# Kernel tuning notes

Measured on AMD Instinct MI355X. Metric: run time of the kernel, lower is better.

The kernel has to match this reference:

```python
import jax, jax.numpy as jnp
import numpy as np

B = 65536
N_HOSTS = 16
N_FEATS = 48        # 3 * n_hosts
N_WINDOW = 3
N_LATENT = 10
GAT_IN = 3
GAT_OUT = 16
E = N_WINDOW + GAT_OUT  # 19, MHA embed dim
PROTO_DIM = 10


def setup_inputs() -> dict:
    key = jax.random.key(0)
    ks = jax.random.split(key, 20)
    def rn(k, shape, scale=0.1):
        return jax.random.normal(k, shape, dtype=jnp.float32) * scale
    return {
        "t": jax.random.normal(ks[0], (B, N_WINDOW, N_FEATS), dtype=jnp.float32),
        "s": jnp.zeros((1,), jnp.float32),  # unused by forward, kept for signature fidelity
        "h0": jax.random.normal(ks[1], (B, 1, N_WINDOW), dtype=jnp.float32),
        "gru_Wih": rn(ks[2], (3 * N_WINDOW, N_FEATS)),
        "gru_Whh": rn(ks[3], (3 * N_WINDOW, N_WINDOW)),
        "gru_bih": rn(ks[4], (3 * N_WINDOW,)),
        "gru_bhh": rn(ks[5], (3 * N_WINDOW,)),
        "gat_W": rn(ks[6], (GAT_IN, GAT_OUT)),
        "gat_al": rn(ks[7], (GAT_OUT,)),
        "gat_ar": rn(ks[8], (GAT_OUT,)),
        "mha_Win": rn(ks[9], (3 * E, E)),
        "mha_bin": rn(ks[10], (3 * E,)),
        "mha_Wout": rn(ks[11], (E, E)),
        "mha_bout": rn(ks[12], (E,)),
        "enc_W": rn(ks[13], (N_HOSTS * N_LATENT, N_WINDOW * E)),
        "enc_b": rn(ks[14], (N_HOSTS * N_LATENT,)),
        "anom_W": rn(ks[15], (2, N_LATENT)),
        "anom_b": rn(ks[16], (2,)),
        "proto_W": rn(ks[17], (PROTO_DIM, N_LATENT)),
        "proto_b": rn(ks[18], (PROTO_DIM,)),
    }


def _forward(t, s, h0, gru_Wih, gru_Whh, gru_bih, gru_bhh,
             gat_W, gat_al, gat_ar, mha_Win, mha_bin, mha_Wout, mha_bout,
             enc_W, enc_b, anom_W, anom_b, proto_W, proto_b):
    # ---- GRU (seq-first, batch B, hidden = n_window = 3) ----
    xs = jnp.swapaxes(t, 0, 1)  # (3, B, 48)
    h0_ = h0[:, 0, :]           # (B, 3)

    def gru_step(h, x_t):
        gi = x_t @ gru_Wih.T + gru_bih   # (B, 9)
        gh = h @ gru_Whh.T + gru_bhh     # (B, 9)
        i_r, i_z, i_n = jnp.split(gi, 3, axis=-1)
        h_r, h_z, h_n = jnp.split(gh, 3, axis=-1)
        r = jax.nn.sigmoid(i_r + h_r)
        z = jax.nn.sigmoid(i_z + h_z)
        n = jnp.tanh(i_n + r * h_n)
        h_new = (1.0 - z) * n + z * h
        return h_new, h_new

    _, gru_out = jax.lax.scan(gru_step, h0_, xs)  # (3, B, 3)

    # ---- GAT on fully-connected 16-node graph (with self loops) ----
    gin = t.reshape(t.shape[0], N_WINDOW, N_HOSTS, GAT_IN)      # (B, 3, 16, 3)
    z = jnp.einsum("bwnc,cf->bwnf", gin, gat_W)                 # (B, 3, 16, 16)
    el = z @ gat_al                                              # src scores (B,3,16)
    er = z @ gat_ar                                              # dst scores (B,3,16)
    e = jax.nn.leaky_relu(er[..., :, None] + el[..., None, :], 0.2)  # (B,3,v,u)
    alpha = jax.nn.softmax(e, axis=-1)                           # softmax over sources u
    gat_nodes = jnp.einsum("bwvu,bwuf->bwvf", alpha, z)          # (B, 3, 16, 16)
    gat_out = gat_nodes.mean(axis=2)                             # (B, 3, 16) mean over hosts
    gat_out = jnp.swapaxes(gat_out, 0, 1)                        # (3, B, 16)

    # ---- concat + single-head MHA (embed=19) ----
    c = jnp.concatenate([gru_out, gat_out], axis=-1)             # (3, B, 19)
    Wq, Wk, Wv = jnp.split(mha_Win, 3, axis=0)
    bq, bk, bv = jnp.split(mha_bin, 3, axis=0)
    q = c @ Wq.T + bq
    k = c @ Wk.T + bk
    v = c @ Wv.T + bv
    scores = jnp.einsum("sbe,tbe->bst", q, k) / jnp.sqrt(jnp.float32(E))
    attw = jax.nn.softmax(scores, axis=-1)
    attn = jnp.einsum("bst,tbe->sbe", attw, v)
    attn = attn @ mha_Wout.T + mha_bout                          # (3, B, 19)

    # ---- encoder: Linear(57,160); LeakyReLU(True) => negative_slope=1.0 => identity ----
    flat = jnp.swapaxes(attn, 0, 1).reshape(-1, N_WINDOW * E)    # (B, 57), seq-major flatten
    latent = flat @ enc_W.T + enc_b                              # (B, 160)
    latent = latent.reshape(-1, N_HOSTS, N_LATENT)               # (B, 16, 10)

    # ---- per-host tiny decoders, vectorized ----
    anomaly = jax.nn.softmax(latent @ anom_W.T + anom_b, axis=-1)   # (B, 16, 2)
    proto = jax.nn.sigmoid(latent @ proto_W.T + proto_b)            # (B, 16, PROTO_DIM)
    return anomaly, proto


def reference(t, s, h0, gru_Wih, gru_Whh, gru_bih, gru_bhh,
              gat_W, gat_al, gat_ar, mha_Win, mha_bin, mha_Wout, mha_bout,
              enc_W, enc_b, anom_W, anom_b, proto_W, proto_b):
    return _forward(t, s, h0, gru_Wih, gru_Whh, gru_bih, gru_bhh,
                    gat_W, gat_al, gat_ar, mha_Win, mha_bin, mha_Wout, mha_bout,
                    enc_W, enc_b, anom_W, anom_b, proto_W, proto_b)
```

## Files before the change

### kernel.cpp

```cpp
#include <hip/hip_runtime.h>

#define NW 3
#define NF 48
#define NHOST 16
#define NLAT 10
#define GOUT 16
#define EDIM 19
#define PDIM 10

#define CB_M    0
#define CB_P    361
#define CB_G    722
#define CB_H    741
#define CB_R    760
#define CB_C0   779
#define CB_WAL  780
#define CB_WAR  783
#define CB_CBIG 800
#define CB_BF   976
#define CB_TOT  10240

typedef __attribute__((ext_vector_type(8))) short bf16x8;
typedef __attribute__((ext_vector_type(4))) float f32x4;

__device__ __forceinline__ float frcp(float x){ return __builtin_amdgcn_rcpf(x); }
__device__ __forceinline__ float fsig(float x){ return frcp(1.f + __expf(-x)); }
__device__ __forceinline__ float ftanh(float x){ return 1.f - 2.f*frcp(1.f + __expf(2.f*x)); }
__device__ __forceinline__ unsigned short f2bf(float x){
    union { float f; unsigned u; } v; v.f = x;
    unsigned r = v.u + 0x7FFFu + ((v.u >> 16) & 1u);
    return (unsigned short)(r >> 16);
}

__global__ __launch_bounds__(256) void k_const(
    const float* __restrict__ Win, const float* __restrict__ bin,
    const float* __restrict__ Wout, const float* __restrict__ bout,
    const float* __restrict__ gatW, const float* __restrict__ gal,
    const float* __restrict__ gar, const float* __restrict__ encW,
    const float* __restrict__ encb,
    const float* __restrict__ aW, const float* __restrict__ ab,
    const float* __restrict__ pW, const float* __restrict__ pb,
    float* __restrict__ cb)
{
    const int w = blockIdx.x*blockDim.x + threadIdx.x;
    if (w < 786) {
        const int idx = w;
        float acc = 0.f;
        if (idx < 361) {
            int i = idx/19, j = idx%19;
            for (int e = 0; e < EDIM; ++e) acc += Win[e*EDIM+i]*Win[(EDIM+e)*EDIM+j];
        } else if (idx < 722) {
            int k = idx-361; int i = k/19, j = k%19;
            for (int e = 0; e < EDIM; ++e) acc += Wout[i*EDIM+e]*Win[(2*EDIM+e)*EDIM+j];
        } else if (idx < 741) {
            int j = idx-722;
            for (int e = 0; e < EDIM; ++e) acc += bin[e]*Win[(EDIM+e)*EDIM+j];
        } else if (idx < 760) {
            int i = idx-741;
            for (int e = 0; e < EDIM; ++e) acc += Win[e*EDIM+i]*bin[EDIM+e];
        } else if (idx < 779) {
            int i = idx-760; acc = bout[i];
            for (int e = 0; e < EDIM; ++e) acc += Wout[i*EDIM+e]*bin[2*EDIM+e];
        } else if (idx == 779) {
            for (int e = 0; e < EDIM; ++e) acc += bin[e]*bin[EDIM+e];
        } else {
            int c = idx-780; int cc = c%3; bool left = c<3;
            for (int f2 = 0; f2 < GOUT; ++f2)
                acc += gatW[cc*GOUT+f2]*(left ? gal[f2] : gar[f2]);
        }
        cb[idx] = acc;
    } else if (w < 962) {
        const int g = w - 786;
        int host = g / 11, jj = g % 11;
        float acc = (jj == 0) ? (ab[0] - ab[1]) : pb[jj-1];
        for (int l = 0; l < NLAT; ++l) {
            float coef = (jj == 0) ? (aW[l] - aW[NLAT+l]) : pW[(jj-1)*NLAT + l];
            acc += coef * encb[host*NLAT + l];
        }
        cb[CB_CBIG + g] = acc;
    } else if (w < 12226) {
        unsigned short* bf = (unsigned short*)(cb + CB_BF);
        const int u = w - 962;
        int j    = u & 7;
        int lane = (u >> 3) & 63;
        int tile = u >> 9;
        int half = tile / 11, n = tile % 11;
        int k = half*32 + ((lane >> 4) & 3)*8 + j;
        int g = n*16 + (lane & 15);
        float acc = 0.f;
        if (k < 57) {
            int host = g / 11, jj = g % 11;
            for (int l = 0; l < NLAT; ++l) {
                float coef = (jj == 0) ? (aW[l] - aW[NLAT+l]) : pW[(jj-1)*NLAT + l];
                acc += coef * encW[(host*NLAT + l)*57 + k];
            }
        }
        bf[u] = f2bf(acc);
    }
}

__global__ __launch_bounds__(256) void k_front(
    const float* __restrict__ t, const float* __restrict__ Wih, const float* __restrict__ bih,
    const float* __restrict__ gatW, const float* __restrict__ cb,
    float* __restrict__ ws1, int B)
{
    const int b = blockIdx.x*blockDim.x + threadIdx.x;
    const int w = blockIdx.y;
    if (b >= B) return;

    float x[NF];
    const float* tp = t + ((size_t)b*NW + w)*NF;
#pragma unroll
    for (int i = 0; i < NF/4; ++i) {
        float4 v = *reinterpret_cast<const float4*>(tp + i*4);
        x[i*4+0]=v.x; x[i*4+1]=v.y; x[i*4+2]=v.z; x[i*4+3]=v.w;
    }
    float* o = ws1 + (size_t)w*25*B + b;
#pragma unroll
    for (int r = 0; r < 9; ++r) {
        float acc = bih[r];
#pragma unroll
        for (int j = 0; j < NF; ++j) acc += x[j]*Wih[r*NF+j];
        o[(size_t)r*B] = acc;
    }
    const float Wal0=cb[CB_WAL],Wal1=cb[CB_WAL+1],Wal2=cb[CB_WAL+2];
    const float War0=cb[CB_WAR],War1=cb[CB_WAR+1],War2=cb[CB_WAR+2];
    float el[NHOST], er[NHOST];
#pragma unroll
    for (int n = 0; n < NHOST; ++n) {
        el[n] = x[n*3+0]*Wal0 + x[n*3+1]*Wal1 + x[n*3+2]*Wal2;
        er[n] = x[n*3+0]*War0 + x[n*3+1]*War1 + x[n*3+2]*War2;
    }
    float beta[NHOST];
#pragma unroll
    for (int u = 0; u < NHOST; ++u) beta[u] = 0.f;
#pragma unroll
    for (int v = 0; v < NHOST; ++v) {
        float ee[NHOST]; float sum = 0.f;
#pragma unroll
        for (int u = 0; u < NHOST; ++u) {
            float s = er[v] + el[u];
            s = fmaxf(s, 0.2f*s);
            ee[u] = __expf(s); sum += ee[u];
        }
        float inv = frcp(sum);
#pragma unroll
        for (int u = 0; u < NHOST; ++u) beta[u] += ee[u]*inv;
    }
    float g0=0.f, g1=0.f, g2=0.f;
#pragma unroll
    for (int u = 0; u < NHOST; ++u) {
        float bu = beta[u]*(1.f/16.f);
        g0 += bu*x[u*3+0]; g1 += bu*x[u*3+1]; g2 += bu*x[u*3+2];
    }
#pragma unroll
    for (int f2 = 0; f2 < GOUT; ++f2)
        o[(size_t)(9+f2)*B] = g0*gatW[f2] + g1*gatW[GOUT+f2] + g2*gatW[2*GOUT+f2];
}

__global__ __launch_bounds__(192) void k_m(
    const float* __restrict__ ws1, const float* __restrict__ h0,
    const float* __restrict__ Whh, const float* __restrict__ bhh,
    const float* __restrict__ cb, unsigned short* __restrict__ ws2bf, int B)
{
    __shared__ float mtb[NW][EDIM][64];
    __shared__ float gtb[NW][64];
    __shared__ float pcb[NW][EDIM][64];
    const int bl = threadIdx.x & 63;
    const int s  = threadIdx.x >> 6;
    const int b  = blockIdx.x*64 + bl;

    float h[3] = { h0[(size_t)b*3+0], h0[(size_t)b*3+1], h0[(size_t)b*3+2] };
    float ch[NW][3];
#pragma unroll
    for (int w = 0; w < NW; ++w) {
        float gi[9];
#pragma unroll
        for (int r = 0; r < 9; ++r) gi[r] = ws1[((size_t)w*25 + r)*B + b];
        float gh[9];
#pragma unroll
        for (int r = 0; r < 9; ++r)
            gh[r] = bhh[r] + h[0]*Whh[r*3+0] + h[1]*Whh[r*3+1] + h[2]*Whh[r*3+2];
#pragma unroll
        for (int j = 0; j < 3; ++j) {
            float rg = fsig(gi[j]   + gh[j]);
            float zg = fsig(gi[3+j] + gh[3+j]);
            float ng = ftanh(gi[6+j] + rg*gh[6+j]);
            h[j] = (1.f - zg)*ng + zg*h[j];
        }
        ch[w][0]=h[0]; ch[w][1]=h[1]; ch[w][2]=h[2];
    }
    float cw[EDIM];
#pragma unroll
    for (int j = 0; j < 3; ++j)
        cw[j] = (s==0) ? ch[0][j] : (s==1) ? ch[1][j] : ch[2][j];
#pragma unroll
    for (int f2 = 0; f2 < GOUT; ++f2)
        cw[3+f2] = ws1[((size_t)s*25 + 9 + f2)*B + b];

    float hsv = 0.f, gt = 0.f;
#pragma unroll
    for (int i = 0; i < EDIM; ++i) { hsv += cw[i]*cb[CB_H+i]; gt += cw[i]*cb[CB_G+i]; }
#pragma unroll
    for (int i = 0; i < EDIM; ++i) {
        float a = 0.f;
#pragma unroll
        for (int j = 0; j < EDIM; ++j) a += cb[CB_M+i*EDIM+j]*cw[j];
        mtb[s][i][bl] = a;
    }
    gtb[s][bl] = gt;
    __syncthreads();

    const float c0 = cb[CB_C0];
    float sc[NW];
#pragma unroll
    for (int tt = 0; tt < NW; ++tt) {
        float a = 0.f;
#pragma unroll
        for (int i = 0; i < EDIM; ++i) a += cw[i]*mtb[tt][i][bl];
        sc[tt] = (a + gtb[tt][bl] + hsv + c0) * 0.2294157338705618f;
    }
    float m = fmaxf(sc[0], fmaxf(sc[1], sc[2]));
    float e0=__expf(sc[0]-m), e1=__expf(sc[1]-m), e2=__expf(sc[2]-m);
    float inv = frcp(e0+e1+e2);
    float aw0=e0*inv, aw1=e1*inv, aw2=e2*inv;

#pragma unroll
    for (int i = 0; i < EDIM; ++i) {
        float a = 0.f;
#pragma unroll
        for (int j = 0; j < EDIM; ++j) a += cb[CB_P+i*EDIM+j]*cw[j];
        pcb[s][i][bl] = a;
    }
    __syncthreads();

    unsigned short* ob = ws2bf + (size_t)b*64 + s*EDIM;
#pragma unroll
    for (int i = 0; i < EDIM; ++i) {
        float v = cb[CB_R+i] + aw0*pcb[0][i][bl] + aw1*pcb[1][i][bl]
                + aw2*pcb[2][i][bl];
        ob[i] = f2bf(v);
    }
    if (s == 0) {
        unsigned short* pz = ws2bf + (size_t)b*64 + 57;
#pragma unroll
        for (int r = 0; r < 7; ++r) pz[r] = 0;
    }
}

__global__ __launch_bounds__(256) void k_enc(
    const unsigned short* __restrict__ ws2bf, const float* __restrict__ cb,
    float* __restrict__ outA, float* __restrict__ outP, int B)
{
    __shared__ float lg[64][178];
    const int lane = threadIdx.x & 63;
    const int wv   = __builtin_amdgcn_readfirstlane(threadIdx.x >> 6);
    const int b0   = blockIdx.x*64;
    if (b0 >= B) return;

    const int brow = b0 + wv*16 + (lane & 15);
    const int koff = (lane >> 4) * 8;
    const unsigned short* ap = ws2bf + (size_t)brow*64;
    union { uint4 q; bf16x8 v; } a0, a1;
    a0.q = *reinterpret_cast<const uint4*>(ap + koff);
    a1.q = *reinterpret_cast<const uint4*>(ap + 32 + koff);

    const uint4* bfq = (const uint4*)(cb + CB_BF);
    const int r0 = wv*16 + ((lane >> 4) << 2);
#pragma unroll
    for (int n = 0; n < 11; ++n) {
        union { uint4 q; bf16x8 v; } bf0, bf1;
        bf0.q = bfq[(size_t)n*64 + lane];
        bf1.q = bfq[(size_t)(11 + n)*64 + lane];
        f32x4 acc = {0.f, 0.f, 0.f, 0.f};
        acc = __builtin_amdgcn_mfma_f32_16x16x32_bf16(a0.v, bf0.v, acc, 0, 0, 0);
        acc = __builtin_amdgcn_mfma_f32_16x16x32_bf16(a1.v, bf1.v, acc, 0, 0, 0);
        const int c = n*16 + (lane & 15);
#pragma unroll
        for (int r = 0; r < 4; ++r) lg[r0 + r][c] = acc[r];
    }
    __syncthreads();

    const int host = threadIdx.x & 15;
    const int tg   = threadIdx.x >> 4;
    const float* cbig = cb + CB_CBIG;
#pragma unroll
    for (int i = 0; i < 4; ++i) {
        const int bl = tg + 16*i;
        const int b  = b0 + bl;
        float v[11];
#pragma unroll
        for (int jj = 0; jj < 11; ++jj)
            v[jj] = lg[bl][host*11 + jj] + cbig[host*11 + jj];
        float p0 = fsig(v[0]);
        float2 av; av.x = p0; av.y = 1.f - p0;
        *reinterpret_cast<float2*>(outA + (size_t)b*32 + host*2) = av;
        float* pP = outP + (size_t)b*160 + host*10;
#pragma unroll
        for (int p = 0; p < 5; ++p) {
            float2 pv; pv.x = fsig(v[1 + 2*p]); pv.y = fsig(v[2 + 2*p]);
            *reinterpret_cast<float2*>(pP + 2*p) = pv;
        }
    }
}

extern "C" void kernel_launch(void* const* d_in, const int* in_sizes, int n_in,
                              void* d_out, int out_size, void* d_ws, size_t ws_size,
                              hipStream_t stream) {
    const float* t    = (const float*)d_in[0];
    const float* h0   = (const float*)d_in[2];
    const float* Wih  = (const float*)d_in[3];
    const float* Whh  = (const float*)d_in[4];
    const float* bih  = (const float*)d_in[5];
    const float* bhh  = (const float*)d_in[6];
    const float* gatW = (const float*)d_in[7];
    const float* gal  = (const float*)d_in[8];
    const float* gar  = (const float*)d_in[9];
    const float* Win  = (const float*)d_in[10];
    const float* bin  = (const float*)d_in[11];
    const float* Wout = (const float*)d_in[12];
    const float* bout = (const float*)d_in[13];
    const float* encW = (const float*)d_in[14];
    const float* encb = (const float*)d_in[15];
    const float* aW   = (const float*)d_in[16];
    const float* ab   = (const float*)d_in[17];
    const float* pW   = (const float*)d_in[18];
    const float* pb   = (const float*)d_in[19];

    const int B = in_sizes[0] / (NW * NF);
    float* cb  = (float*)d_ws;
    float* ws1 = cb + CB_TOT;
    unsigned short* ws2bf = (unsigned short*)(ws1 + (size_t)25*NW*B);
    float* outA = (float*)d_out;
    float* outP = (float*)d_out + (size_t)B*32;

    k_const<<<dim3(48), 256, 0, stream>>>(Win, bin, Wout, bout, gatW, gal, gar,
                                          encW, encb, aW, ab, pW, pb, cb);
    k_front<<<dim3((B+255)/256, NW), 256, 0, stream>>>(t, Wih, bih, gatW, cb, ws1, B);
    k_m<<<dim3(B/64), 192, 0, stream>>>(ws1, h0, Whh, bhh, cb, ws2bf, B);
    k_enc<<<dim3((B+63)/64), 256, 0, stream>>>(ws2bf, cb, outA, outP, B);
}
```

Measured before the change: 73.20 us.

## Fuse front, attention, and encoder kernels into one block-local kernel

Merges the GRU/GAT front kernel, the attention kernel, and the MFMA encoder kernel into one kernel per 64-row tile. Intermediates move through LDS (with an XOR-swizzled bf16 A tile) instead of global workspace buffers. This removes two launches and the global round trips of the ws1 and ws2bf intermediates. In exchange it uses about 64KB of LDS per block, which limits occupancy, and a quarter of the threads sit idle during the front stages.

```diff
diff --git a/kernel.cpp b/kernel.cpp
--- a/kernel.cpp
+++ b/kernel.cpp
@@ -99,207 +99,239 @@
     }
 }
 
-__global__ __launch_bounds__(256) void k_front(
-    const float* __restrict__ t, const float* __restrict__ Wih, const float* __restrict__ bih,
-    const float* __restrict__ gatW, const float* __restrict__ cb,
-    float* __restrict__ ws1, int B)
-{
-    const int b = blockIdx.x*blockDim.x + threadIdx.x;
-    const int w = blockIdx.y;
-    if (b >= B) return;
-
-    float x[NF];
-    const float* tp = t + ((size_t)b*NW + w)*NF;
-#pragma unroll
-    for (int i = 0; i < NF/4; ++i) {
-        float4 v = *reinterpret_cast<const float4*>(tp + i*4);
-        x[i*4+0]=v.x; x[i*4+1]=v.y; x[i*4+2]=v.z; x[i*4+3]=v.w;
-    }
-    float* o = ws1 + (size_t)w*25*B + b;
-#pragma unroll
-    for (int r = 0; r < 9; ++r) {
-        float acc = bih[r];
-#pragma unroll
-        for (int j = 0; j < NF; ++j) acc += x[j]*Wih[r*NF+j];
-        o[(size_t)r*B] = acc;
-    }
-    const float Wal0=cb[CB_WAL],Wal1=cb[CB_WAL+1],Wal2=cb[CB_WAL+2];
-    const float War0=cb[CB_WAR],War1=cb[CB_WAR+1],War2=cb[CB_WAR+2];
-    float el[NHOST], er[NHOST];
-#pragma unroll
-    for (int n = 0; n < NHOST; ++n) {
-        el[n] = x[n*3+0]*Wal0 + x[n*3+1]*Wal1 + x[n*3+2]*Wal2;
-        er[n] = x[n*3+0]*War0 + x[n*3+1]*War1 + x[n*3+2]*War2;
-    }
-    float beta[NHOST];
-#pragma unroll
-    for (int u = 0; u < NHOST; ++u) beta[u] = 0.f;
-#pragma unroll
-    for (int v = 0; v < NHOST; ++v) {
-        float ee[NHOST]; float sum = 0.f;
-#pragma unroll
-        for (int u = 0; u < NHOST; ++u) {
-            float s = er[v] + el[u];
-            s = fmaxf(s, 0.2f*s);
-            ee[u] = __expf(s); sum += ee[u];
-        }
-        float inv = frcp(sum);
-#pragma unroll
-        for (int u = 0; u < NHOST; ++u) beta[u] += ee[u]*inv;
-    }
-    float g0=0.f, g1=0.f, g2=0.f;
-#pragma unroll
-    for (int u = 0; u < NHOST; ++u) {
-        float bu = beta[u]*(1.f/16.f);
-        g0 += bu*x[u*3+0]; g1 += bu*x[u*3+1]; g2 += bu*x[u*3+2];
-    }
-#pragma unroll
-    for (int f2 = 0; f2 < GOUT; ++f2)
-        o[(size_t)(9+f2)*B] = g0*gatW[f2] + g1*gatW[GOUT+f2] + g2*gatW[2*GOUT+f2];
-}
-
-__global__ __launch_bounds__(192) void k_m(
-    const float* __restrict__ ws1, const float* __restrict__ h0,
-    const float* __restrict__ Whh, const float* __restrict__ bhh,
-    const float* __restrict__ cb, unsigned short* __restrict__ ws2bf, int B)
-{
-    __shared__ float mtb[NW][EDIM][64];
-    __shared__ float gtb[NW][64];
-    __shared__ float pcb[NW][EDIM][64];
-    const int bl = threadIdx.x & 63;
-    const int s  = threadIdx.x >> 6;
-    const int b  = blockIdx.x*64 + bl;
-
-    float h[3] = { h0[(size_t)b*3+0], h0[(size_t)b*3+1], h0[(size_t)b*3+2] };
-    float ch[NW][3];
-#pragma unroll
-    for (int w = 0; w < NW; ++w) {
-        float gi[9];
-#pragma unroll
-        for (int r = 0; r < 9; ++r) gi[r] = ws1[((size_t)w*25 + r)*B + b];
-        float gh[9];
-#pragma unroll
-        for (int r = 0; r < 9; ++r)
-            gh[r] = bhh[r] + h[0]*Whh[r*3+0] + h[1]*Whh[r*3+1] + h[2]*Whh[r*3+2];
-#pragma unroll
-        for (int j = 0; j < 3; ++j) {
-            float rg = fsig(gi[j]   + gh[j]);
-            float zg = fsig(gi[3+j] + gh[3+j]);
-            float ng = ftanh(gi[6+j] + rg*gh[6+j]);
-            h[j] = (1.f - zg)*ng + zg*h[j];
-        }
-        ch[w][0]=h[0]; ch[w][1]=h[1]; ch[w][2]=h[2];
-    }
-    float cw[EDIM];
-#pragma unroll
-    for (int j = 0; j < 3; ++j)
-        cw[j] = (s==0) ? ch[0][j] : (s==1) ? ch[1][j] : ch[2][j];
-#pragma unroll
-    for (int f2 = 0; f2 < GOUT; ++f2)
-        cw[3+f2] = ws1[((size_t)s*25 + 9 + f2)*B + b];
-
-    float hsv = 0.f, gt = 0.f;
-#pragma unroll
-    for (int i = 0; i < EDIM; ++i) { hsv += cw[i]*cb[CB_H+i]; gt += cw[i]*cb[CB_G+i]; }
-#pragma unroll
-    for (int i = 0; i < EDIM; ++i) {
-        float a = 0.f;
-#pragma unroll
-        for (int j = 0; j < EDIM; ++j) a += cb[CB_M+i*EDIM+j]*cw[j];
-        mtb[s][i][bl] = a;
-    }
-    gtb[s][bl] = gt;
-    __syncthreads();
-
-    const float c0 = cb[CB_C0];
-    float sc[NW];
-#pragma unroll
-    for (int tt = 0; tt < NW; ++tt) {
-        float a = 0.f;
-#pragma unroll
-        for (int i = 0; i < EDIM; ++i) a += cw[i]*mtb[tt][i][bl];
-        sc[tt] = (a + gtb[tt][bl] + hsv + c0) * 0.2294157338705618f;
-    }
-    float m = fmaxf(sc[0], fmaxf(sc[1], sc[2]));
-    float e0=__expf(sc[0]-m), e1=__expf(sc[1]-m), e2=__expf(sc[2]-m);
-    float inv = frcp(e0+e1+e2);
-    float aw0=e0*inv, aw1=e1*inv, aw2=e2*inv;
-
-#pragma unroll
-    for (int i = 0; i < EDIM; ++i) {
-        float a = 0.f;
-#pragma unroll
-        for (int j = 0; j < EDIM; ++j) a += cb[CB_P+i*EDIM+j]*cw[j];
-        pcb[s][i][bl] = a;
-    }
-    __syncthreads();
-
-    unsigned short* ob = ws2bf + (size_t)b*64 + s*EDIM;
-#pragma unroll
-    for (int i = 0; i < EDIM; ++i) {
-        float v = cb[CB_R+i] + aw0*pcb[0][i][bl] + aw1*pcb[1][i][bl]
-                + aw2*pcb[2][i][bl];
-        ob[i] = f2bf(v);
-    }
-    if (s == 0) {
-        unsigned short* pz = ws2bf + (size_t)b*64 + 57;
-#pragma unroll
-        for (int r = 0; r < 7; ++r) pz[r] = 0;
-    }
-}
-
-__global__ __launch_bounds__(256) void k_enc(
-    const unsigned short* __restrict__ ws2bf, const float* __restrict__ cb,
+__global__ __launch_bounds__(256) void k_fused(
+    const float* __restrict__ t, const float* __restrict__ h0,
+    const float* __restrict__ Wih, const float* __restrict__ bih,
+    const float* __restrict__ gatW, const float* __restrict__ Whh,
+    const float* __restrict__ bhh, const float* __restrict__ cb,
     float* __restrict__ outA, float* __restrict__ outP, int B)
 {
-    __shared__ float lg[64][178];
-    const int lane = threadIdx.x & 63;
-    const int wv   = __builtin_amdgcn_readfirstlane(threadIdx.x >> 6);
-    const int b0   = blockIdx.x*64;
-    if (b0 >= B) return;
-
-    const int brow = b0 + wv*16 + (lane & 15);
-    const int koff = (lane >> 4) * 8;
-    const unsigned short* ap = ws2bf + (size_t)brow*64;
-    union { uint4 q; bf16x8 v; } a0, a1;
-    a0.q = *reinterpret_cast<const uint4*>(ap + koff);
-    a1.q = *reinterpret_cast<const uint4*>(ap + 32 + koff);
-
-    const uint4* bfq = (const uint4*)(cb + CB_BF);
-    const int r0 = wv*16 + ((lane >> 4) << 2);
-#pragma unroll
-    for (int n = 0; n < 11; ++n) {
-        union { uint4 q; bf16x8 v; } bf0, bf1;
-        bf0.q = bfq[(size_t)n*64 + lane];
-        bf1.q = bfq[(size_t)(11 + n)*64 + lane];
-        f32x4 acc = {0.f, 0.f, 0.f, 0.f};
-        acc = __builtin_amdgcn_mfma_f32_16x16x32_bf16(a0.v, bf0.v, acc, 0, 0, 0);
-        acc = __builtin_amdgcn_mfma_f32_16x16x32_bf16(a1.v, bf1.v, acc, 0, 0, 0);
-        const int c = n*16 + (lane & 15);
-#pragma unroll
-        for (int r = 0; r < 4; ++r) lg[r0 + r][c] = acc[r];
-    }
-    __syncthreads();
-
-    const int host = threadIdx.x & 15;
-    const int tg   = threadIdx.x >> 4;
-    const float* cbig = cb + CB_CBIG;
-#pragma unroll
-    for (int i = 0; i < 4; ++i) {
-        const int bl = tg + 16*i;
-        const int b  = b0 + bl;
-        float v[11];
-#pragma unroll
-        for (int jj = 0; jj < 11; ++jj)
-            v[jj] = lg[bl][host*11 + jj] + cbig[host*11 + jj];
-        float p0 = fsig(v[0]);
-        float2 av; av.x = p0; av.y = 1.f - p0;
-        *reinterpret_cast<float2*>(outA + (size_t)b*32 + host*2) = av;
-        float* pP = outP + (size_t)b*160 + host*10;
-#pragma unroll
-        for (int p = 0; p < 5; ++p) {
-            float2 pv; pv.x = fsig(v[1 + 2*p]); pv.y = fsig(v[2 + 2*p]);
-            *reinterpret_cast<float2*>(pP + 2*p) = pv;
+    __shared__ __align__(16) char smraw[57344];
+    __shared__ __align__(16) unsigned short a2[64][64];
+    float (*fm)[25][64] = reinterpret_cast<float(*)[25][64]>(smraw);
+    float* xs            = reinterpret_cast<float*>(smraw + 19200);
+    float (*mtb)[EDIM][64] = reinterpret_cast<float(*)[EDIM][64]>(smraw + 19200);
+    float (*gtb)[64]       = reinterpret_cast<float(*)[64]>(smraw + 19200 + 14592);
+    float (*pcb)[EDIM][64] = reinterpret_cast<float(*)[EDIM][64]>(smraw + 19200 + 15360);
+    float (*lg)[178]       = reinterpret_cast<float(*)[178]>(smraw);
+
+    const int tid = threadIdx.x;
+    const int b0  = blockIdx.x * 64;
+    const int bl  = tid & 63;
+    const int sw  = tid >> 6;
+
+    if (tid < 192) {
+        const int w = sw;
+        const float* tp = t + ((size_t)(b0 + bl)*NW + w)*NF;
+        float* xrow = xs + tid*49;
+
+        const float Wal0=cb[CB_WAL],Wal1=cb[CB_WAL+1],Wal2=cb[CB_WAL+2];
+        const float War0=cb[CB_WAR],War1=cb[CB_WAR+1],War2=cb[CB_WAR+2];
+
+        float gi[9];
+#pragma unroll
+        for (int r = 0; r < 9; ++r) gi[r] = bih[r];
+        float el[NHOST], er[NHOST];
+#pragma unroll
+        for (int c = 0; c < 4; ++c) {
+            float xc[12];
+#pragma unroll
+            for (int i = 0; i < 3; ++i) {
+                float4 v = *reinterpret_cast<const float4*>(tp + c*12 + i*4);
+                xc[i*4+0]=v.x; xc[i*4+1]=v.y; xc[i*4+2]=v.z; xc[i*4+3]=v.w;
+            }
+#pragma unroll
+            for (int k = 0; k < 12; ++k) xrow[c*12 + k] = xc[k];
+#pragma unroll
+            for (int r = 0; r < 9; ++r) {
+                float a = 0.f;
+#pragma unroll
+                for (int k = 0; k < 12; ++k) a += xc[k]*Wih[r*NF + c*12 + k];
+                gi[r] += a;
+            }
+#pragma unroll
+            for (int u = 0; u < 4; ++u) {
+                const int uu = c*4 + u;
+                el[uu] = xc[u*3]*Wal0 + xc[u*3+1]*Wal1 + xc[u*3+2]*Wal2;
+                er[uu] = xc[u*3]*War0 + xc[u*3+1]*War1 + xc[u*3+2]*War2;
+            }
+        }
+#pragma unroll
+        for (int r = 0; r < 9; ++r) fm[w][r][bl] = gi[r];
+
+        float beta[NHOST];
+#pragma unroll
+        for (int u = 0; u < NHOST; ++u) beta[u] = 0.f;
+#pragma unroll
+        for (int v = 0; v < NHOST; ++v) {
+            float ee[NHOST]; float sum = 0.f;
+#pragma unroll
+            for (int u = 0; u < NHOST; ++u) {
+                float s = er[v] + el[u];
+                s = fmaxf(s, 0.2f*s);
+                ee[u] = __expf(s); sum += ee[u];
+            }
+            float inv = frcp(sum);
+#pragma unroll
+            for (int u = 0; u < NHOST; ++u) beta[u] += ee[u]*inv;
+        }
+        float g0=0.f, g1=0.f, g2=0.f;
+#pragma unroll
+        for (int u = 0; u < NHOST; ++u) {
+            float bu = beta[u]*(1.f/16.f);
+            g0 += bu*xrow[u*3+0]; g1 += bu*xrow[u*3+1]; g2 += bu*xrow[u*3+2];
+        }
+#pragma unroll
+        for (int f2 = 0; f2 < GOUT; ++f2)
+            fm[w][9+f2][bl] = g0*gatW[f2] + g1*gatW[GOUT+f2] + g2*gatW[2*GOUT+f2];
+    }
+    __syncthreads();
+
+    float cw[EDIM];
+    float hsv = 0.f, aw0 = 0.f, aw1 = 0.f, aw2 = 0.f;
+#pragma unroll
+    for (int i = 0; i < EDIM; ++i) cw[i] = 0.f;
+
+    if (tid < 192) {
+        const int s = sw;
+        const int b = b0 + bl;
+        float h[3] = { h0[(size_t)b*3+0], h0[(size_t)b*3+1], h0[(size_t)b*3+2] };
+        float ch[NW][3];
+#pragma unroll
+        for (int w = 0; w < NW; ++w) {
+            float gi[9];
+#pragma unroll
+            for (int r = 0; r < 9; ++r) gi[r] = fm[w][r][bl];
+            float gh[9];
+#pragma unroll
+            for (int r = 0; r < 9; ++r)
+                gh[r] = bhh[r] + h[0]*Whh[r*3+0] + h[1]*Whh[r*3+1] + h[2]*Whh[r*3+2];
+#pragma unroll
+            for (int j = 0; j < 3; ++j) {
+                float rg = fsig(gi[j]   + gh[j]);
+                float zg = fsig(gi[3+j] + gh[3+j]);
+                float ng = ftanh(gi[6+j] + rg*gh[6+j]);
+                h[j] = (1.f - zg)*ng + zg*h[j];
+            }
+            ch[w][0]=h[0]; ch[w][1]=h[1]; ch[w][2]=h[2];
+        }
+#pragma unroll
+        for (int j = 0; j < 3; ++j)
+            cw[j] = (s==0) ? ch[0][j] : (s==1) ? ch[1][j] : ch[2][j];
+#pragma unroll
+        for (int f2 = 0; f2 < GOUT; ++f2)
+            cw[3+f2] = fm[s][9+f2][bl];
+
+        float gt = 0.f;
+#pragma unroll
+        for (int i = 0; i < EDIM; ++i) { hsv += cw[i]*cb[CB_H+i]; gt += cw[i]*cb[CB_G+i]; }
+#pragma unroll
+        for (int i = 0; i < EDIM; ++i) {
+            float a = 0.f;
+#pragma unroll
+            for (int j = 0; j < EDIM; ++j) a += cb[CB_M+i*EDIM+j]*cw[j];
+            mtb[s][i][bl] = a;
+        }
+        gtb[s][bl] = gt;
+    }
+    __syncthreads();
+
+    if (tid < 192) {
+        const int s = sw;
+        const float c0 = cb[CB_C0];
+        float sc[NW];
+#pragma unroll
+        for (int tt = 0; tt < NW; ++tt) {
+            float a = 0.f;
+#pragma unroll
+            for (int i = 0; i < EDIM; ++i) a += cw[i]*mtb[tt][i][bl];
+            sc[tt] = (a + gtb[tt][bl] + hsv + c0) * 0.2294157338705618f;
+        }
+        float m = fmaxf(sc[0], fmaxf(sc[1], sc[2]));
+        float e0=__expf(sc[0]-m), e1=__expf(sc[1]-m), e2=__expf(sc[2]-m);
+        float inv = frcp(e0+e1+e2);
+        aw0=e0*inv; aw1=e1*inv; aw2=e2*inv;
+
+#pragma unroll
+        for (int i = 0; i < EDIM; ++i) {
+            float a = 0.f;
+#pragma unroll
+            for (int j = 0; j < EDIM; ++j) a += cb[CB_P+i*EDIM+j]*cw[j];
+            pcb[s][i][bl] = a;
+        }
+    }
+    __syncthreads();
+
+    if (tid < 192) {
+        const int s = sw;
+        char* a2c = (char*)a2;
+        const int swz = (bl & 7) << 4;
+#pragma unroll
+        for (int i = 0; i < EDIM; ++i) {
+            float v = cb[CB_R+i] + aw0*pcb[0][i][bl] + aw1*pcb[1][i][bl]
+                    + aw2*pcb[2][i][bl];
+            const int byte = bl*128 + (s*EDIM + i)*2;
+            *reinterpret_cast<unsigned short*>(a2c + (byte ^ swz)) = f2bf(v);
+        }
+        if (s == 0) {
+#pragma unroll
+            for (int r = 0; r < 7; ++r) {
+                const int byte = bl*128 + (57 + r)*2;
+                *reinterpret_cast<unsigned short*>(a2c + (byte ^ swz)) = 0;
+            }
+        }
+    }
+    __syncthreads();
+
+    const int lane = tid & 63;
+    const int wv   = __builtin_amdgcn_readfirstlane(sw);
+    {
+        const int browl = wv*16 + (lane & 15);
+        const int koff  = (lane >> 4) * 8;
+        const char* a2c = (const char*)a2;
+        const int swz = (browl & 7) << 4;
+        union { uint4 q; bf16x8 v; } a0, a1;
+        a0.q = *reinterpret_cast<const uint4*>(a2c + ((browl*128 + koff*2) ^ swz));
+        a1.q = *reinterpret_cast<const uint4*>(a2c + ((browl*128 + 64 + koff*2) ^ swz));
+
+        const uint4* bfq = (const uint4*)(cb + CB_BF);
+        const int r0 = wv*16 + ((lane >> 4) << 2);
+#pragma unroll
+        for (int n = 0; n < 11; ++n) {
+            union { uint4 q; bf16x8 v; } bf0, bf1;
+            bf0.q = bfq[(size_t)n*64 + lane];
+            bf1.q = bfq[(size_t)(11 + n)*64 + lane];
+            f32x4 acc = {0.f, 0.f, 0.f, 0.f};
+            acc = __builtin_amdgcn_mfma_f32_16x16x32_bf16(a0.v, bf0.v, acc, 0, 0, 0);
+            acc = __builtin_amdgcn_mfma_f32_16x16x32_bf16(a1.v, bf1.v, acc, 0, 0, 0);
+            const int c = n*16 + (lane & 15);
+#pragma unroll
+            for (int r = 0; r < 4; ++r) lg[r0 + r][c] = acc[r];
+        }
+    }
+    __syncthreads();
+
+    {
+        const int host = tid & 15;
+        const int tg   = tid >> 4;
+        const float* cbig = cb + CB_CBIG;
+#pragma unroll
+        for (int i = 0; i < 4; ++i) {
+            const int bll = tg + 16*i;
+            const int b   = b0 + bll;
+            float v[11];
+#pragma unroll
+            for (int jj = 0; jj < 11; ++jj)
+                v[jj] = lg[bll][host*11 + jj] + cbig[host*11 + jj];
+            float p0 = fsig(v[0]);
+            float2 av; av.x = p0; av.y = 1.f - p0;
+            *reinterpret_cast<float2*>(outA + (size_t)b*32 + host*2) = av;
+            float* pP = outP + (size_t)b*160 + host*10;
+#pragma unroll
+            for (int p = 0; p < 5; ++p) {
+                float2 pv; pv.x = fsig(v[1 + 2*p]); pv.y = fsig(v[2 + 2*p]);
+                *reinterpret_cast<float2*>(pP + 2*p) = pv;
+            }
         }
     }
 }
@@ -329,14 +361,11 @@
 
     const int B = in_sizes[0] / (NW * NF);
     float* cb  = (float*)d_ws;
-    float* ws1 = cb + CB_TOT;
-    unsigned short* ws2bf = (unsigned short*)(ws1 + (size_t)25*NW*B);
     float* outA = (float*)d_out;
     float* outP = (float*)d_out + (size_t)B*32;
 
     k_const<<<dim3(48), 256, 0, stream>>>(Win, bin, Wout, bout, gatW, gal, gar,
                                           encW, encb, aW, ab, pW, pb, cb);
-    k_front<<<dim3((B+255)/256, NW), 256, 0, stream>>>(t, Wih, bih, gatW, cb, ws1, B);
-    k_m<<<dim3(B/64), 192, 0, stream>>>(ws1, h0, Whh, bhh, cb, ws2bf, B);
-    k_enc<<<dim3((B+63)/64), 256, 0, stream>>>(ws2bf, cb, outA, outP, B);
+    k_fused<<<dim3(B/64), 256, 0, stream>>>(t, h0, Wih, bih, gatW, Whh, bhh, cb,
+                                            outA, outP, B);
 }
```

Measured after the change: 64.97 us (median of 2 runs). 11.2% less time.
